# Kernel tuning notes

Hardware: AMD Instinct MI355X
Metric: run time of the kernel (lower is better)

## Reference

```python
import jax, jax.numpy as jnp
import numpy as np

B, C_IN, H, W = 2, 128, 96, 320
CQ = C_IN // 4   # q/k channels = 32
D = 32           # number of disparities


def _groupnorm1(x, w, b, eps=1e-5):
    # GroupNorm with 1 group == LayerNorm over (C,H,W) per sample, per-channel affine
    mu = x.mean(axis=(1, 2, 3), keepdims=True)
    var = x.var(axis=(1, 2, 3), keepdims=True)
    return (x - mu) / jnp.sqrt(var + eps) * w[None, :, None, None] + b[None, :, None, None]


def _warp_volume(x, disp, directs):
    # Faithful to affine_grid + grid_sample(bilinear, border, align_corners=True)
    # with a pure horizontal shift: pixel offset = disp * direct * (W-1).
    Bx, C, Hx, Wx = x.shape
    d = directs.reshape(Bx, 1, 1)                       # [B,1,1]
    j = jnp.arange(Wx, dtype=x.dtype)
    pos = j[None, None, :] + disp[None, :, None] * d * (Wx - 1)   # [B,D,W]
    pos = jnp.clip(pos, 0.0, Wx - 1)                    # border padding
    x0 = jnp.clip(jnp.floor(pos).astype(jnp.int32), 0, Wx - 1)
    x1 = jnp.minimum(x0 + 1, Wx - 1)
    t = pos - x0.astype(x.dtype)                        # [B,D,W]

    def per_b(xb, i0, i1, tb):
        g0 = xb[:, :, i0]                                # [C,H,D,W]
        g1 = xb[:, :, i1]
        return g0 * (1.0 - tb) + g1 * tb

    warped = jax.vmap(per_b)(x, x0, x1, t)               # [B,C,H,D,W]
    return jnp.moveaxis(warped, 3, 4)                    # [B,C,H,W,D]


def setup_inputs() -> dict:
    key = jax.random.key(0)
    ks = jax.random.split(key, 12)
    s = lambda i, shape: jax.random.normal(ks[i], shape, jnp.float32) * 0.05
    return {
        "t_feat": jax.random.normal(ks[0], (B, C_IN, H, W), jnp.float32),
        "s_feat": jax.random.normal(ks[1], (B, C_IN, H, W), jnp.float32),
        "directs": jnp.ones((B, 1, 1, 1), jnp.float32),
        "disp": jnp.arange(D, dtype=jnp.float32) * 0.01,   # norm_disp_range
        "q_w": s(2, (CQ, C_IN)), "q_b": jnp.zeros((CQ,), jnp.float32),
        "k_w": s(3, (CQ, C_IN)), "k_b": jnp.zeros((CQ,), jnp.float32),
        "cf_w": s(4, (1, 1, 3, 3, 3)), "cf_b": jnp.zeros((1,), jnp.float32),
        "nt_w": jnp.ones((C_IN,), jnp.float32), "nt_b": jnp.zeros((C_IN,), jnp.float32),
        "nc_w": jnp.ones((D,), jnp.float32), "nc_b": jnp.zeros((D,), jnp.float32),
        "ce_w": s(5, (C_IN, D)), "ce_b": jnp.zeros((C_IN,), jnp.float32),
        "fa_w": s(6, (1, 2 * C_IN)), "fa_b": jnp.zeros((1,), jnp.float32),
        "rc_w": s(7, (C_IN, C_IN, 3, 3)), "rc_b": jnp.zeros((C_IN,), jnp.float32),
        "se_w1": s(8, (C_IN // 16, C_IN)),
        "se_w2": s(9, (C_IN, C_IN // 16)),
    }


def reference(t_feat, s_feat, directs, disp, q_w, q_b, k_w, k_b, cf_w, cf_b,
              nt_w, nt_b, nc_w, nc_b, ce_w, ce_b, fa_w, fa_b, rc_w, rc_b,
              se_w1, se_w2):
    eps = 1e-12
    # 1x1 q/k projections
    q = jnp.einsum('oc,bchw->bohw', q_w, t_feat) + q_b[None, :, None, None]
    k = jnp.einsum('oc,bchw->bohw', k_w, s_feat) + k_b[None, :, None, None]

    # per-disparity warp -> [B,Cq,H,W,D]
    warped = _warp_volume(k, disp, directs)

    # DAV with patch_size=1: per-pixel cosine similarity over channels
    qn = q / jnp.maximum(jnp.linalg.norm(q, axis=1, keepdims=True), eps)
    kn = warped / jnp.maximum(jnp.linalg.norm(warped, axis=1, keepdims=True), eps)
    sim = jnp.einsum('bchw,bchwd->bdhw', qn, kn)          # [B,D,H,W]

    # 3x3x3 cost filter (Conv3d 1->1, padding 1)
    cost = jax.lax.conv_general_dilated(
        sim[:, None], cf_w, (1, 1, 1), [(1, 1)] * 3,
        dimension_numbers=('NCDHW', 'OIDHW', 'NCDHW'))[:, 0] + cf_b[0]
    norm_cost = jax.nn.softmax(cost, axis=1)              # softmax over D

    t_n = _groupnorm1(t_feat, nt_w, nt_b)
    c_n = _groupnorm1(norm_cost, nc_w, nc_b)
    cost_feat = jnp.einsum('od,bdhw->bohw', ce_w, c_n) + ce_b[None, :, None, None]

    fusion_in = jnp.concatenate([t_n, cost_feat], axis=1)
    alpha = jax.nn.sigmoid(jnp.einsum('oc,bchw->bohw', fa_w, fusion_in)
                           + fa_b[None, :, None, None])
    fused = alpha * t_n + (1.0 - alpha) * cost_feat       # same spatial size, no interp

    # redu: reflection-pad 3x3 conv -> SE -> ELU
    xp = jnp.pad(fused, ((0, 0), (0, 0), (1, 1), (1, 1)), mode='reflect')
    x = jax.lax.conv_general_dilated(
        xp, rc_w, (1, 1), 'VALID',
        dimension_numbers=('NCHW', 'OIHW', 'NCHW')) + rc_b[None, :, None, None]
    y = x.mean(axis=(2, 3))                               # [B,C]
    y = jax.nn.relu(y @ se_w1.T)
    y = jax.nn.sigmoid(y @ se_w2.T)
    x = jax.nn.elu(x * y[:, :, None, None])
    return (x, norm_cost)
```

## Files before the change

### kernel.cpp

```cpp
#include <hip/hip_runtime.h>
#include <stdint.h>

#define CC    128
#define CQn   32
#define DD    32
#define IMG_H 96
#define IMG_W 320
#define HW    30720
#define NPIX  61440

#define OFF_Q     0
#define OFF_K     3932160
#define OFF_SIM   7864320
#define OFF_NCP   15728640
#define OFF_FUSED 0
#define OFF_WC    19660800
#define OFF_WQK   19955712
#define OFF_AP    19972096
#define OFF_MISC  19988480
#define OFF_ST    20000768

typedef _Float16 half_t;
typedef _Float16 f16x2 __attribute__((ext_vector_type(2)));
typedef _Float16 f16x8 __attribute__((ext_vector_type(8)));
typedef float    f32x4 __attribute__((ext_vector_type(4)));

__device__ __forceinline__ float fdot2f(f16x2 a, f16x2 b, float c){
#if __has_builtin(__builtin_amdgcn_fdot2)
  return __builtin_amdgcn_fdot2(a, b, c, false);
#else
  return c + (float)a.x*(float)b.x + (float)a.y*(float)b.y;
#endif
}

__global__ __launch_bounds__(256) void k0_prep(
    const float* __restrict__ rc_w, const float* __restrict__ q_w, const float* __restrict__ k_w,
    const float* __restrict__ ce_w, const float* __restrict__ ce_b,
    const float* __restrict__ fa_w, const float* __restrict__ nt_w, const float* __restrict__ nt_b,
    half_t* __restrict__ wconv, half_t* __restrict__ wqk, float* __restrict__ gbuf){
  int blk = blockIdx.x, tid = threadIdx.x;
  if (blk < 576){
    int idx = blk * 256 + tid;
    int j = idx & 7;
    int o = (idx >> 3) & 127;
    int g = idx >> 10;
    int kq = g & 3, q4 = (g >> 2) & 3, pos = g >> 4;
    int c = q4*32 + kq*8 + j;
    wconv[idx] = (half_t)rc_w[(o*128 + c)*9 + pos];
  } else if (blk < 608){
    int idx = (blk - 576) * 256 + tid;
    wqk[idx] = (half_t)(idx < 4096 ? q_w[idx] : k_w[idx - 4096]);
  } else {
    int t = tid;
    if (t < 32){
      float a = 0.f;
      for (int o = 0; o < 128; o++) a += fa_w[128 + o] * ce_w[o * 32 + t];
      gbuf[t] = a;
    } else if (t == 32){
      float a = 0.f;
      for (int o = 0; o < 128; o++) a += fa_w[128 + o] * ce_b[o];
      gbuf[32] = a;
    } else if (t == 33){
      float a = 0.f;
      for (int c = 0; c < 128; c++) a += fa_w[c] * nt_w[c];
      gbuf[33] = a;
    } else if (t == 34){
      float a = 0.f;
      for (int c = 0; c < 128; c++) a += fa_w[c] * nt_b[c];
      gbuf[34] = a;
    }
  }
}

__global__ __launch_bounds__(256) void k1_qk(
    const float* __restrict__ t_feat, const float* __restrict__ s_feat,
    const half_t* __restrict__ wqk, const float* __restrict__ q_b, const float* __restrict__ k_b,
    half_t* __restrict__ qbuf, half_t* __restrict__ kbuf,
    double* __restrict__ tsum, double* __restrict__ tsq){
  __shared__ half_t feat[128 * 136];
  __shared__ float red1[4], red2[4];
  __shared__ float qbl[32], kbl[32];
  int tid = threadIdx.x;
  int b = blockIdx.x / 240;
  int pix0 = (blockIdx.x % 240) * 128;
  int lane = tid & 63, wid = tid >> 6;
  int quad = lane >> 4, l15 = lane & 15;
  if (tid < 32){ qbl[tid] = q_b[tid]; kbl[tid] = k_b[tid]; }
  int px_s = tid & 127, hf = tid >> 7;

  for (int phase = 0; phase < 2; phase++){
    const float* src = (phase == 0 ? t_feat : s_feat) + (size_t)b * CC * HW + pix0 + px_s;
    float s1 = 0.f, s2 = 0.f;
    for (int c = hf * 64; c < hf * 64 + 64; c += 2){
      float v0 = src[c * HW], v1 = src[(c + 1) * HW];
      if (phase == 0){ s1 += v0 + v1; s2 += v0 * v0 + v1 * v1; }
      *(f16x2*)&feat[px_s * 136 + c] = f16x2{(half_t)v0, (half_t)v1};
    }
    if (phase == 0){
      #pragma unroll
      for (int off = 32; off > 0; off >>= 1){ s1 += __shfl_down(s1, off, 64); s2 += __shfl_down(s2, off, 64); }
      if (lane == 0){ red1[wid] = s1; red2[wid] = s2; }
    }
    __syncthreads();
    if (phase == 0 && tid == 0){
      atomicAdd(&tsum[b], (double)red1[0] + red1[1] + red1[2] + red1[3]);
      atomicAdd(&tsq[b],  (double)red2[0] + red2[1] + red2[2] + red2[3]);
    }
    const half_t* W = wqk + phase * 4096;
    f32x4 acc[2][2];
    #pragma unroll
    for (int m = 0; m < 2; m++){ acc[m][0] = (f32x4){0,0,0,0}; acc[m][1] = (f32x4){0,0,0,0}; }
    #pragma unroll
    for (int q4 = 0; q4 < 4; q4++){
      f16x8 a0 = *(const f16x8*)&W[(l15) * 128 + q4*32 + quad*8];
      f16x8 a1 = *(const f16x8*)&W[(16 + l15) * 128 + q4*32 + quad*8];
      #pragma unroll
      for (int nt = 0; nt < 2; nt++){
        f16x8 bf = *(const f16x8*)&feat[(wid*32 + nt*16 + l15) * 136 + q4*32 + quad*8];
        acc[0][nt] = __builtin_amdgcn_mfma_f32_16x16x32_f16(a0, bf, acc[0][nt], 0, 0, 0);
        acc[1][nt] = __builtin_amdgcn_mfma_f32_16x16x32_f16(a1, bf, acc[1][nt], 0, 0, 0);
      }
    }
    const float* bl = phase == 0 ? qbl : kbl;
    #pragma unroll
    for (int m = 0; m < 2; m++)
      #pragma unroll
      for (int nt = 0; nt < 2; nt++)
        #pragma unroll
        for (int r = 0; r < 4; r++){
          int o = m*16 + quad*4 + r;
          feat[(wid*32 + nt*16 + l15) * 136 + o] = (half_t)(acc[m][nt][r] + bl[o]);
        }
    __syncthreads();
    {
      half_t* dst = (phase == 0 ? qbuf : kbuf) + (size_t)(b * HW + pix0 + px_s) * 32;
      if (hf == 0){
        uint4* d4 = (uint4*)dst;
        const uint4* s4 = (const uint4*)&feat[px_s * 136];
        d4[0] = s4[0]; d4[1] = s4[1]; d4[2] = s4[2]; d4[3] = s4[3];
      }
    }
    __syncthreads();
  }
}

__global__ __launch_bounds__(640) void k2_sim(
    const half_t* __restrict__ qbuf, const half_t* __restrict__ kbuf,
    const float* __restrict__ directs, const float* __restrict__ disp,
    float* __restrict__ sim){
  __shared__ uint4 klds4[320 * 5];
  __shared__ float displ[32];
  int tid = threadIdx.x;
  int b = blockIdx.y, h = blockIdx.x;
  for (int u = tid; u < 1280; u += 640){
    int x = u >> 2, j = u & 3;
    klds4[x * 5 + j] = ((const uint4*)(kbuf + (size_t)(b * HW + h * IMG_W + x) * 32))[j];
  }
  if (tid < 32) displ[tid] = disp[tid];
  __syncthreads();
  int dh = tid >= 320 ? 1 : 0;
  int w = tid - dh * 320;
  int d0 = dh * 16;
  float direct = directs[b];
  union U16 { uint4 u4[4]; f16x2 h2[16]; };
  U16 qu;
  {
    const uint4* qp = (const uint4*)(qbuf + (size_t)(b * HW + h * IMG_W + w) * 32);
    qu.u4[0] = qp[0]; qu.u4[1] = qp[1]; qu.u4[2] = qp[2]; qu.u4[3] = qp[3];
  }
  float nq2 = 0.f;
  #pragma unroll
  for (int i = 0; i < 16; i++) nq2 = fdot2f(qu.h2[i], qu.h2[i], nq2);
  float inv_q = 1.0f / fmaxf(sqrtf(nq2), 1e-12f);
  float* simb = sim + (size_t)b * DD * HW + h * IMG_W + w;
  for (int d = d0; d < d0 + 16; d++){
    float pos = (float)w + displ[d] * direct * (float)(IMG_W - 1);
    pos = fminf(fmaxf(pos, 0.0f), (float)(IMG_W - 1));
    int x0 = (int)pos;
    int x1 = min(x0 + 1, IMG_W - 1);
    half_t tt = (half_t)(pos - (float)x0);
    f16x2 t2 = {tt, tt};
    U16 k0u, k1u;
    const uint4* r0 = &klds4[x0 * 5];
    const uint4* r1 = &klds4[x1 * 5];
    #pragma unroll
    for (int j = 0; j < 4; j++){ k0u.u4[j] = r0[j]; k1u.u4[j] = r1[j]; }
    float dot = 0.f, n2 = 0.f;
    #pragma unroll
    for (int i = 0; i < 16; i++){
      f16x2 wv = k0u.h2[i] + t2 * (k1u.h2[i] - k0u.h2[i]);
      dot = fdot2f(wv, qu.h2[i], dot);
      n2  = fdot2f(wv, wv, n2);
    }
    simb[d * HW] = dot * inv_q / fmaxf(sqrtf(n2), 1e-12f);
  }
}

__global__ __launch_bounds__(320) void k3_cost(
    const float* __restrict__ sim, const float* __restrict__ cf_w,
    float* __restrict__ norm_cost, half_t* __restrict__ ncp,
    double* __restrict__ csum, double* __restrict__ csq){
  __shared__ float w3[27];
  __shared__ float red1[5], red2[5];
  int tid = threadIdx.x;
  if (tid < 27) w3[tid] = cf_w[tid];
  __syncthreads();
  int b = blockIdx.y, h = blockIdx.x, w = tid;
  float cost[32];
  #pragma unroll
  for (int d = 0; d < 32; d++) cost[d] = 0.f;
  const float* sb = sim + (size_t)b * DD * HW;
  #pragma unroll
  for (int i = 0; i < 3; i++){
    int hh = h + i - 1;
    if (hh < 0 || hh >= IMG_H) continue;
    #pragma unroll
    for (int j = 0; j < 3; j++){
      int ww = w + j - 1;
      bool ok = (ww >= 0 && ww < IMG_W);
      const float* col = sb + hh * IMG_W + (ok ? ww : 0);
      float w0 = w3[0*9 + i*3 + j], w1 = w3[1*9 + i*3 + j], w2 = w3[2*9 + i*3 + j];
      #pragma unroll
      for (int e = 0; e < 32; e++){
        float v = ok ? col[e * HW] : 0.f;
        if (e < 31) cost[e+1] += w0 * v;
        cost[e] += w1 * v;
        if (e > 0)  cost[e-1] += w2 * v;
      }
    }
  }
  float mx = cost[0];
  #pragma unroll
  for (int d = 1; d < 32; d++) mx = fmaxf(mx, cost[d]);
  float s = 0.f;
  #pragma unroll
  for (int d = 0; d < 32; d++){ cost[d] = expf(cost[d] - mx); s += cost[d]; }
  float inv = 1.0f / s;
  float s1 = 0.f, s2 = 0.f;
  float* nb = norm_cost + (size_t)b * DD * HW + h * IMG_W + w;
  #pragma unroll
  for (int d = 0; d < 32; d++){
    float nc = cost[d] * inv;
    cost[d] = nc;
    nb[d * HW] = nc;
    s1 += nc; s2 += nc * nc;
  }
  {
    union { f16x2 h2[16]; uint4 u4[4]; } u;
    #pragma unroll
    for (int i = 0; i < 16; i++) u.h2[i] = f16x2{(half_t)cost[2*i], (half_t)cost[2*i+1]};
    uint4* dst = (uint4*)(ncp + (size_t)(b * HW + h * IMG_W + w) * 32);
    dst[0] = u.u4[0]; dst[1] = u.u4[1]; dst[2] = u.u4[2]; dst[3] = u.u4[3];
  }
  #pragma unroll
  for (int off = 32; off > 0; off >>= 1){ s1 += __shfl_down(s1, off, 64); s2 += __shfl_down(s2, off, 64); }
  int lane = tid & 63, wid = tid >> 6;
  if (lane == 0){ red1[wid] = s1; red2[wid] = s2; }
  __syncthreads();
  if (tid == 0){
    double a1 = 0, a2 = 0;
    for (int i = 0; i < 5; i++){ a1 += red1[i]; a2 += red2[i]; }
    atomicAdd(&csum[b], a1);
    atomicAdd(&csq[b], a2);
  }
}

__global__ __launch_bounds__(256) void k35_prep(
    const float* __restrict__ ce_w, const float* __restrict__ ce_b,
    const float* __restrict__ nt_w, const float* __restrict__ nt_b,
    const float* __restrict__ nc_w, const float* __restrict__ nc_b,
    const float* __restrict__ fa_w, const float* __restrict__ fa_b,
    const double* __restrict__ tsum, const double* __restrict__ tsq,
    const double* __restrict__ csum, const double* __restrict__ csq,
    const float* __restrict__ gbuf, half_t* __restrict__ ap, float* __restrict__ biasp,
    float* __restrict__ tnA, float* __restrict__ tnB, float* __restrict__ h1g,
    float* __restrict__ gp, float* __restrict__ zc){
  int t = threadIdx.x;
  int b = t >> 7, o = t & 127;
  float mu_t  = (float)(tsum[b] * (1.0 / (128.0 * HW)));
  float var_t = (float)(tsq[b]  * (1.0 / (128.0 * HW))) - mu_t * mu_t;
  float inv_t = 1.0f / sqrtf(var_t + 1e-5f);
  float mu_c  = (float)(csum[b] * (1.0 / (32.0 * HW)));
  float var_c = (float)(csq[b]  * (1.0 / (32.0 * HW))) - mu_c * mu_c;
  float inv_c = 1.0f / sqrtf(var_c + 1e-5f);
  float bias = ce_b[o];
  half_t* apo = ap + (size_t)(b * 128 + o) * 32;
  for (int d = 0; d < 32; d++){
    float wv = ce_w[o * 32 + d];
    bias += wv * (nc_b[d] - nc_w[d] * inv_c * mu_c);
    apo[d] = (half_t)(wv * nc_w[d] * inv_c);
  }
  biasp[b * 128 + o] = bias;
  tnA[b * 128 + o] = inv_t * nt_w[o];
  tnB[b * 128 + o] = nt_b[o] - mu_t * inv_t * nt_w[o];
  h1g[b * 128 + o] = fa_w[o] * nt_w[o] * inv_t;
  if (o < 32) gp[b * 32 + o] = gbuf[o] * nc_w[o] * inv_c;
  if (o == 0){
    float z = gbuf[32] + gbuf[34] - mu_t * inv_t * gbuf[33] + fa_b[0];
    for (int d = 0; d < 32; d++) z += gbuf[d] * (nc_b[d] - nc_w[d] * inv_c * mu_c);
    zc[b] = z;
  }
}

__global__ __launch_bounds__(256) void k4_fuse(
    const float* __restrict__ t_feat, const half_t* __restrict__ ncp,
    const half_t* __restrict__ ap, const float* __restrict__ biasp,
    const float* __restrict__ tnA, const float* __restrict__ tnB,
    const float* __restrict__ h1g, const float* __restrict__ gp,
    const float* __restrict__ zc, half_t* __restrict__ fused){
  __shared__ half_t cf[128 * 136];
  __shared__ half_t tnb[128 * 136];
  __shared__ float alphas[128];
  __shared__ float zred[256];
  __shared__ float biasl[128], tnAl[128], tnBl[128];
  int tid = threadIdx.x;
  int b = blockIdx.x / 240;
  int pix0 = (blockIdx.x % 240) * 128;
  int lane = tid & 63, wid = tid >> 6, quad = lane >> 4, l15 = lane & 15;
  if (tid < 128){
    biasl[tid] = biasp[b * 128 + tid];
    tnAl[tid] = tnA[b * 128 + tid];
    tnBl[tid] = tnB[b * 128 + tid];
  }
  __syncthreads();
  {
    int px = tid & 127, hf = tid >> 7;
    const float* tf = t_feat + (size_t)b * CC * HW + pix0 + px;
    const float* hg = h1g + b * 128;
    float z = 0.f;
    for (int c = hf * 64; c < hf * 64 + 64; c++){
      float tv = tf[c * HW];
      z += hg[c] * tv;
      tnb[px * 136 + c] = (half_t)(tv * tnAl[c] + tnBl[c]);
    }
    if (hf == 0){
      const half_t* np = ncp + (size_t)(b * HW + pix0 + px) * 32;
      for (int d = 0; d < 32; d++) z += gp[b * 32 + d] * (float)np[d];
    }
    zred[tid] = z;
  }
  __syncthreads();
  if (tid < 128){
    float z = zred[tid] + zred[tid + 128] + zc[b];
    alphas[tid] = 1.0f / (1.0f + expf(-z));
  }
  f32x4 acc[8][2];
  #pragma unroll
  for (int mt = 0; mt < 8; mt++){ acc[mt][0] = (f32x4){0,0,0,0}; acc[mt][1] = (f32x4){0,0,0,0}; }
  f16x8 bfr[2];
  #pragma unroll
  for (int nt = 0; nt < 2; nt++)
    bfr[nt] = *(const f16x8*)&ncp[(size_t)(b * HW + pix0 + wid*32 + nt*16 + l15) * 32 + quad * 8];
  #pragma unroll
  for (int mt = 0; mt < 8; mt++){
    f16x8 a = *(const f16x8*)&ap[(size_t)(b * 128 + mt*16 + l15) * 32 + quad * 8];
    acc[mt][0] = __builtin_amdgcn_mfma_f32_16x16x32_f16(a, bfr[0], acc[mt][0], 0, 0, 0);
    acc[mt][1] = __builtin_amdgcn_mfma_f32_16x16x32_f16(a, bfr[1], acc[mt][1], 0, 0, 0);
  }
  __syncthreads();
  #pragma unroll
  for (int nt = 0; nt < 2; nt++){
    int px = wid*32 + nt*16 + l15;
    float al = alphas[px];
    #pragma unroll
    for (int mt = 0; mt < 8; mt++)
      #pragma unroll
      for (int r = 0; r < 4; r++){
        int o = mt*16 + quad*4 + r;
        float cfv = acc[mt][nt][r] + biasl[o];
        float tn = (float)tnb[px * 136 + o];
        cf[px * 136 + o] = (half_t)(al * (tn - cfv) + cfv);
      }
  }
  __syncthreads();
  {
    int px = tid >> 1, hf = tid & 1;
    const uint4* srow = (const uint4*)&cf[px * 136 + hf * 64];
    uint4* drow = (uint4*)(fused + (size_t)(b * HW + pix0 + px) * 128 + hf * 64);
    #pragma unroll
    for (int j = 0; j < 8; j++) drow[j] = srow[j];
  }
}

__global__ __launch_bounds__(256, 2) void k5_conv(
    const half_t* __restrict__ fused, const half_t* __restrict__ wconv,
    const float* __restrict__ rc_b, float* __restrict__ xout, float* __restrict__ ysum){
  __shared__ __align__(16) half_t patch[16][6][34][8];
  __shared__ float rcb[128];
  int tid = threadIdx.x;
  int b = blockIdx.z;
  int h0 = blockIdx.y * 4;
  int w0 = blockIdx.x * 32;
  int lane = tid & 63, wid = tid >> 6, quad = lane >> 4, l15 = lane & 15;
  int oh = wid >> 1, ph = wid & 1;
  if (tid < 128) rcb[tid] = rc_b[tid];

  {
    int j = tid >> 4, pl = tid & 15;
    #pragma unroll
    for (int it = 0; it < 13; it++){
      int pp = it * 16 + pl;
      if (pp < 204){
        int r = pp / 34, col = pp - r * 34;
        int hs = h0 + r - 1;  hs = hs < 0 ? 1 : (hs >= IMG_H ? 2*IMG_H - 2 - hs : hs);
        int ws = w0 + col - 1; ws = ws < 0 ? 1 : (ws >= IMG_W ? 2*IMG_W - 2 - ws : ws);
        *(uint4*)&patch[j][r][col][0] =
            *((const uint4*)(fused + (size_t)(b * HW + hs * IMG_W + ws) * 128) + j);
      }
    }
  }
  __syncthreads();

  f32x4 acc[4][4];
  #pragma unroll
  for (int mt = 0; mt < 4; mt++)
    #pragma unroll
    for (int nt = 0; nt < 4; nt++) acc[mt][nt] = (f32x4){0.f,0.f,0.f,0.f};

  const half_t* wbase = wconv + ((size_t)quad * 128 + oh * 64 + l15) * 8;
  f16x8 Acur[4], Anext[4];
  #pragma unroll
  for (int mt = 0; mt < 4; mt++) Anext[mt] = *(const f16x8*)(wbase + mt * 128);
  for (int s = 0; s < 36; s++){
    #pragma unroll
    for (int mt = 0; mt < 4; mt++) Acur[mt] = Anext[mt];
    if (s < 35){
      const half_t* wp = wbase + (size_t)(s + 1) * 4096;
      #pragma unroll
      for (int mt = 0; mt < 4; mt++) Anext[mt] = *(const f16x8*)(wp + mt * 128);
    }
    int pos = s >> 2, q4 = s & 3;
    int kh = (pos * 11) >> 5;
    int kw = pos - kh * 3;
    #pragma unroll
    for (int nt = 0; nt < 4; nt++){
      f16x8 B = *(const f16x8*)&patch[q4*4 + quad][nt + kh][ph*16 + l15 + kw][0];
      #pragma unroll
      for (int mt = 0; mt < 4; mt++)
        acc[mt][nt] = __builtin_amdgcn_mfma_f32_16x16x32_f16(Acur[mt], B, acc[mt][nt], 0, 0, 0);
    }
  }

  #pragma unroll
  for (int mt = 0; mt < 4; mt++){
    float ysl[4] = {0.f, 0.f, 0.f, 0.f};
    #pragma unroll
    for (int nt = 0; nt < 4; nt++){
      int hh = h0 + nt;
      int ww = w0 + ph*16 + l15;
      #pragma unroll
      for (int r = 0; r < 4; r++){
        int o = oh*64 + mt*16 + quad*4 + r;
        float v = acc[mt][nt][r] + rcb[o];
        xout[((size_t)(b * CC + o) * IMG_H + hh) * IMG_W + ww] = v;
        float rv = v;
        rv += __shfl_xor(rv, 1, 64);
        rv += __shfl_xor(rv, 2, 64);
        rv += __shfl_xor(rv, 4, 64);
        rv += __shfl_xor(rv, 8, 64);
        ysl[r] += rv;
      }
    }
    if (l15 == 0){
      #pragma unroll
      for (int r = 0; r < 4; r++)
        atomicAdd(&ysum[b * CC + oh*64 + mt*16 + quad*4 + r], ysl[r]);
    }
  }
}

__global__ __launch_bounds__(256) void k6_se(
    const float* __restrict__ ysum, const float* __restrict__ se_w1,
    const float* __restrict__ se_w2, float* __restrict__ sescale){
  __shared__ float ym[256];
  __shared__ float y1[16];
  int t = threadIdx.x;
  ym[t] = ysum[t] * (1.0f / (float)HW);
  __syncthreads();
  if (t < 16){
    int b = t >> 3, j = t & 7;
    float a = 0.f;
    for (int o = 0; o < 128; o++) a += ym[b * 128 + o] * se_w1[j * 128 + o];
    y1[t] = fmaxf(a, 0.f);
  }
  __syncthreads();
  int b = t >> 7, o = t & 127;
  float a = 0.f;
  #pragma unroll
  for (int j = 0; j < 8; j++) a += y1[b * 8 + j] * se_w2[o * 8 + j];
  sescale[t] = 1.0f / (1.0f + expf(-a));
}

__global__ __launch_bounds__(256) void k7_elu(float* __restrict__ x, const float* __restrict__ sescale){
  int i4 = blockIdx.x * 256 + threadIdx.x;
  float4* xp = (float4*)x;
  float4 v = xp[i4];
  float s = sescale[i4 / 7680];
  float a = v.x * s, bb = v.y * s, c = v.z * s, d = v.w * s;
  v.x = a  > 0.f ? a  : expm1f(a);
  v.y = bb > 0.f ? bb : expm1f(bb);
  v.z = c  > 0.f ? c  : expm1f(c);
  v.w = d  > 0.f ? d  : expm1f(d);
  xp[i4] = v;
}

extern "C" void kernel_launch(void* const* d_in, const int* in_sizes, int n_in,
                              void* d_out, int out_size, void* d_ws, size_t ws_size,
                              hipStream_t stream){
  const float* t_feat = (const float*)d_in[0];
  const float* s_feat = (const float*)d_in[1];
  const float* directs = (const float*)d_in[2];
  const float* disp   = (const float*)d_in[3];
  const float* q_w = (const float*)d_in[4];
  const float* q_b = (const float*)d_in[5];
  const float* k_w = (const float*)d_in[6];
  const float* k_b = (const float*)d_in[7];
  const float* cf_w = (const float*)d_in[8];
  const float* nt_w = (const float*)d_in[10];
  const float* nt_b = (const float*)d_in[11];
  const float* nc_w = (const float*)d_in[12];
  const float* nc_b = (const float*)d_in[13];
  const float* ce_w = (const float*)d_in[14];
  const float* ce_b = (const float*)d_in[15];
  const float* fa_w = (const float*)d_in[16];
  const float* fa_b = (const float*)d_in[17];
  const float* rc_w = (const float*)d_in[18];
  const float* rc_b = (const float*)d_in[19];
  const float* se_w1 = (const float*)d_in[20];
  const float* se_w2 = (const float*)d_in[21];

  char* ws = (char*)d_ws;
  half_t* qbuf  = (half_t*)(ws + OFF_Q);
  half_t* kbuf  = (half_t*)(ws + OFF_K);
  float*  sim   = (float*)(ws + OFF_SIM);
  half_t* ncp   = (half_t*)(ws + OFF_NCP);
  half_t* fused = (half_t*)(ws + OFF_FUSED);
  half_t* wconv = (half_t*)(ws + OFF_WC);
  half_t* wqk   = (half_t*)(ws + OFF_WQK);
  half_t* ap    = (half_t*)(ws + OFF_AP);
  float*  biasp = (float*)(ws + OFF_MISC);
  float*  tnA   = (float*)(ws + OFF_MISC + 1024);
  float*  tnB   = (float*)(ws + OFF_MISC + 2048);
  float*  h1g   = (float*)(ws + OFF_MISC + 3072);
  float*  gp    = (float*)(ws + OFF_MISC + 4096);
  float*  zc    = (float*)(ws + OFF_MISC + 4352);
  char* st = ws + OFF_ST;
  double* tsum = (double*)(st + 0);
  double* tsq  = (double*)(st + 16);
  double* csum = (double*)(st + 32);
  double* csq  = (double*)(st + 48);
  float* ysum  = (float*)(st + 64);
  float* sescale = (float*)(st + 1088);
  float* gbuf  = (float*)(st + 2112);

  float* xout = (float*)d_out;
  float* norm_cost = (float*)d_out + 7864320;

  hipMemsetAsync(st, 0, 1088, stream);
  k0_prep<<<610, 256, 0, stream>>>(rc_w, q_w, k_w, ce_w, ce_b, fa_w, nt_w, nt_b, wconv, wqk, gbuf);
  k1_qk<<<480, 256, 0, stream>>>(t_feat, s_feat, wqk, q_b, k_b, qbuf, kbuf, tsum, tsq);
  k2_sim<<<dim3(96, 2), 640, 0, stream>>>(qbuf, kbuf, directs, disp, sim);
  k3_cost<<<dim3(96, 2), 320, 0, stream>>>(sim, cf_w, norm_cost, ncp, csum, csq);
  k35_prep<<<1, 256, 0, stream>>>(ce_w, ce_b, nt_w, nt_b, nc_w, nc_b, fa_w, fa_b,
                                  tsum, tsq, csum, csq, gbuf, ap, biasp, tnA, tnB, h1g, gp, zc);
  k4_fuse<<<480, 256, 0, stream>>>(t_feat, ncp, ap, biasp, tnA, tnB, h1g, gp, zc, fused);
  k5_conv<<<dim3(10, 24, 2), 256, 0, stream>>>(fused, wconv, rc_b, xout, ysum);
  k6_se<<<1, 256, 0, stream>>>(ysum, se_w1, se_w2, sescale);
  k7_elu<<<7680, 256, 0, stream>>>(xout, sescale);
}
```

Measured before the change: 324.9 us.

## Shrink conv tile to 16 pixels wide and split output channels across waves

```diff
diff --git a/kernel.cpp b/kernel.cpp
--- a/kernel.cpp
+++ b/kernel.cpp
@@ -382,75 +382,61 @@
   }
 }
 
-__global__ __launch_bounds__(256, 2) void k5_conv(
+__global__ __launch_bounds__(256, 4) void k5_conv(
     const half_t* __restrict__ fused, const half_t* __restrict__ wconv,
     const float* __restrict__ rc_b, float* __restrict__ xout, float* __restrict__ ysum){
-  __shared__ __align__(16) half_t patch[16][6][34][8];
+  __shared__ __align__(16) half_t patch[6 * 18 * 136];
   __shared__ float rcb[128];
   int tid = threadIdx.x;
   int b = blockIdx.z;
   int h0 = blockIdx.y * 4;
-  int w0 = blockIdx.x * 32;
+  int w0 = blockIdx.x * 16;
   int lane = tid & 63, wid = tid >> 6, quad = lane >> 4, l15 = lane & 15;
-  int oh = wid >> 1, ph = wid & 1;
   if (tid < 128) rcb[tid] = rc_b[tid];
 
-  {
-    int j = tid >> 4, pl = tid & 15;
-    #pragma unroll
-    for (int it = 0; it < 13; it++){
-      int pp = it * 16 + pl;
-      if (pp < 204){
-        int r = pp / 34, col = pp - r * 34;
-        int hs = h0 + r - 1;  hs = hs < 0 ? 1 : (hs >= IMG_H ? 2*IMG_H - 2 - hs : hs);
-        int ws = w0 + col - 1; ws = ws < 0 ? 1 : (ws >= IMG_W ? 2*IMG_W - 2 - ws : ws);
-        *(uint4*)&patch[j][r][col][0] =
-            *((const uint4*)(fused + (size_t)(b * HW + hs * IMG_W + ws) * 128) + j);
+  for (int idx = tid; idx < 108 * 16; idx += 256){
+    int pp = idx >> 4, j = idx & 15;
+    int r = pp / 18, col = pp - r * 18;
+    int hs = h0 + r - 1;  hs = hs < 0 ? 1 : (hs >= IMG_H ? 2*IMG_H - 2 - hs : hs);
+    int ws = w0 + col - 1; ws = ws < 0 ? 1 : (ws >= IMG_W ? 2*IMG_W - 2 - ws : ws);
+    const uint4* s = (const uint4*)(fused + (size_t)(b * HW + hs * IMG_W + ws) * 128) + j;
+    *((uint4*)&patch[(r * 18 + col) * 136] + j) = *s;
+  }
+  __syncthreads();
+
+  f32x4 acc[2][4];
+  #pragma unroll
+  for (int mt = 0; mt < 2; mt++)
+    #pragma unroll
+    for (int nt = 0; nt < 4; nt++) acc[mt][nt] = (f32x4){0.f,0.f,0.f,0.f};
+
+  for (int pos = 0; pos < 9; pos++){
+    int kh = pos / 3;
+    int kw2 = pos - kh * 3;
+    #pragma unroll
+    for (int q4 = 0; q4 < 4; q4++){
+      const half_t* wrow = wconv + ((size_t)(pos*16 + q4*4 + quad) * 128 + wid*32 + l15) * 8;
+      f16x8 A0 = *(const f16x8*)wrow;
+      f16x8 A1 = *(const f16x8*)(wrow + 128);
+      #pragma unroll
+      for (int nt = 0; nt < 4; nt++){
+        f16x8 B = *(const f16x8*)&patch[((nt + kh)*18 + l15 + kw2)*136 + q4*32 + quad*8];
+        acc[0][nt] = __builtin_amdgcn_mfma_f32_16x16x32_f16(A0, B, acc[0][nt], 0, 0, 0);
+        acc[1][nt] = __builtin_amdgcn_mfma_f32_16x16x32_f16(A1, B, acc[1][nt], 0, 0, 0);
       }
     }
   }
-  __syncthreads();
-
-  f32x4 acc[4][4];
-  #pragma unroll
-  for (int mt = 0; mt < 4; mt++)
-    #pragma unroll
-    for (int nt = 0; nt < 4; nt++) acc[mt][nt] = (f32x4){0.f,0.f,0.f,0.f};
-
-  const half_t* wbase = wconv + ((size_t)quad * 128 + oh * 64 + l15) * 8;
-  f16x8 Acur[4], Anext[4];
-  #pragma unroll
-  for (int mt = 0; mt < 4; mt++) Anext[mt] = *(const f16x8*)(wbase + mt * 128);
-  for (int s = 0; s < 36; s++){
-    #pragma unroll
-    for (int mt = 0; mt < 4; mt++) Acur[mt] = Anext[mt];
-    if (s < 35){
-      const half_t* wp = wbase + (size_t)(s + 1) * 4096;
-      #pragma unroll
-      for (int mt = 0; mt < 4; mt++) Anext[mt] = *(const f16x8*)(wp + mt * 128);
-    }
-    int pos = s >> 2, q4 = s & 3;
-    int kh = (pos * 11) >> 5;
-    int kw = pos - kh * 3;
-    #pragma unroll
-    for (int nt = 0; nt < 4; nt++){
-      f16x8 B = *(const f16x8*)&patch[q4*4 + quad][nt + kh][ph*16 + l15 + kw][0];
-      #pragma unroll
-      for (int mt = 0; mt < 4; mt++)
-        acc[mt][nt] = __builtin_amdgcn_mfma_f32_16x16x32_f16(Acur[mt], B, acc[mt][nt], 0, 0, 0);
-    }
-  }
-
-  #pragma unroll
-  for (int mt = 0; mt < 4; mt++){
+
+  #pragma unroll
+  for (int mt = 0; mt < 2; mt++){
     float ysl[4] = {0.f, 0.f, 0.f, 0.f};
     #pragma unroll
     for (int nt = 0; nt < 4; nt++){
       int hh = h0 + nt;
-      int ww = w0 + ph*16 + l15;
+      int ww = w0 + l15;
       #pragma unroll
       for (int r = 0; r < 4; r++){
-        int o = oh*64 + mt*16 + quad*4 + r;
+        int o = wid*32 + mt*16 + quad*4 + r;
         float v = acc[mt][nt][r] + rcb[o];
         xout[((size_t)(b * CC + o) * IMG_H + hh) * IMG_W + ww] = v;
         float rv = v;
@@ -464,7 +450,7 @@
     if (l15 == 0){
       #pragma unroll
       for (int r = 0; r < 4; r++)
-        atomicAdd(&ysum[b * CC + oh*64 + mt*16 + quad*4 + r], ysl[r]);
+        atomicAdd(&ysum[b * CC + wid*32 + mt*16 + quad*4 + r], ysl[r]);
     }
   }
 }
@@ -564,7 +550,7 @@
   k35_prep<<<1, 256, 0, stream>>>(ce_w, ce_b, nt_w, nt_b, nc_w, nc_b, fa_w, fa_b,
                                   tsum, tsq, csum, csq, gbuf, ap, biasp, tnA, tnB, h1g, gp, zc);
   k4_fuse<<<480, 256, 0, stream>>>(t_feat, ncp, ap, biasp, tnA, tnB, h1g, gp, zc, fused);
-  k5_conv<<<dim3(10, 24, 2), 256, 0, stream>>>(fused, wconv, rc_b, xout, ysum);
+  k5_conv<<<dim3(20, 24, 2), 256, 0, stream>>>(fused, wconv, rc_b, xout, ysum);
   k6_se<<<1, 256, 0, stream>>>(ysum, se_w1, se_w2, sescale);
   k7_elu<<<7680, 256, 0, stream>>>(xout, sescale);
 }
```

Result: slower. 340.3 us (+4.7%).
